# Optimization experiments

Measured on AMD Instinct MI355X. Metric: run time of the kernel, lower is better.

Reference implementation:

```python
import jax, jax.numpy as jnp
import numpy as np

N, K, D = 100000, 32, 64

def setup_inputs() -> dict:
    key = jax.random.key(0)
    k1, k2, k3 = jax.random.split(key, 3)
    x = jax.random.normal(k1, (N, D), dtype=jnp.float32)
    neighbors = jax.random.randint(k2, (N, K), 0, N, dtype=jnp.int32)
    weights = jax.random.uniform(k3, (N, K), dtype=jnp.float32)
    return {"x": x, "neighbors": neighbors, "weights": weights}

def reference(x, neighbors, weights):
    # Per-node importance pooling: normalize weights over neighbors, then
    # weighted-sum gathered neighbor features. (Vectorized form of the
    # original per-node Python loop; nodes with zero total weight keep
    # unnormalized weights, matching the `if weight_sum > 0` branch.)
    wsum = weights.sum(axis=1, keepdims=True)                 # [N, 1]
    w = jnp.where(wsum > 0, weights / wsum, weights)          # [N, K]
    nbr_feats = x[neighbors]                                  # [N, K, D] gather
    pooled = jnp.einsum("nk,nkd->nd", w, nbr_feats)          # [N, D]
    return pooled
```

## Files before the change

kernel.cpp:

```cpp
#include <hip/hip_runtime.h>
#include <hip/hip_fp16.h>


#define K_NBR 32
#define D_FEAT 64

typedef float f32x4 __attribute__((ext_vector_type(4)));
typedef unsigned int u32x2 __attribute__((ext_vector_type(2)));
typedef unsigned int u32x4 __attribute__((ext_vector_type(4)));

static __device__ __forceinline__ __half2 u32_as_h2(unsigned int u) {
  __half2 h;
  __builtin_memcpy(&h, &u, 4);
  return h;
}

static __device__ __forceinline__ unsigned int h2_as_u32(__half2 h) {
  unsigned int u;
  __builtin_memcpy(&u, &h, 4);
  return u;
}

__global__ __launch_bounds__(256) void ImportancePooling_28424093564958_convert(
    const f32x4* __restrict__ x4, u32x2* __restrict__ xh4, int n4) {
  const int i = blockIdx.x * blockDim.x + threadIdx.x;
  if (i < n4) {
    const f32x4 v = __builtin_nontemporal_load(&x4[i]);
    const __half2 a = __floats2half2_rn(v.x, v.y);
    const __half2 b = __floats2half2_rn(v.z, v.w);
    u32x2 u;
    u.x = h2_as_u32(a);
    u.y = h2_as_u32(b);
    xh4[i] = u;
  }
}

__global__ __launch_bounds__(256, 8) void ImportancePooling_28424093564958_kernel(
    const u32x4* __restrict__ xh4,
    const int* __restrict__ neighbors,
    const float* __restrict__ weights,
    f32x4* __restrict__ out4,
    int Nw) {
  const int wave_id = (int)((blockIdx.x * blockDim.x + threadIdx.x) >> 6);
  const int lane = threadIdx.x & 63;
  if (wave_id >= Nw) return;

  const int g = lane >> 3;
  const int f = lane & 7;
  const int gb4 = g << 2;
  const long hbase = (long)wave_id * 256;

  int wb[4], nb[4];
  {
    const long e0 = hbase + f * 32 + g;
    wb[0] = __float_as_int(__builtin_nontemporal_load(&weights[e0]));
    wb[1] = __float_as_int(__builtin_nontemporal_load(&weights[e0 + 8]));
    wb[2] = __float_as_int(__builtin_nontemporal_load(&weights[e0 + 16]));
    wb[3] = __float_as_int(__builtin_nontemporal_load(&weights[e0 + 24]));
    nb[0] = __builtin_nontemporal_load(&neighbors[e0]);
    nb[1] = __builtin_nontemporal_load(&neighbors[e0 + 8]);
    nb[2] = __builtin_nontemporal_load(&neighbors[e0 + 16]);
    nb[3] = __builtin_nontemporal_load(&neighbors[e0 + 24]);
  }

  float s = __int_as_float(wb[0]) + __int_as_float(wb[1]) +
            __int_as_float(wb[2]) + __int_as_float(wb[3]);
  s += __shfl_xor(s, 8, 64);
  s += __shfl_xor(s, 16, 64);
  s += __shfl_xor(s, 32, 64);
  const float invp = (s > 0.0f) ? (1.0f / s) : 1.0f;
  const float inv = __int_as_float(
      __builtin_amdgcn_ds_bpermute(gb4, __float_as_int(invp)));

  float acc[8];
#pragma unroll
  for (int i = 0; i < 8; ++i) acc[i] = 0.0f;

#pragma unroll
  for (int k = 0; k < K_NBR; ++k) {
    const int addr = ((k & 7) << 5) + gb4;
    const float wk =
        __int_as_float(__builtin_amdgcn_ds_bpermute(addr, wb[k >> 3]));
    const int idx = __builtin_amdgcn_ds_bpermute(addr, nb[k >> 3]);
    const u32x4 h = xh4[(unsigned)idx * 8u + (unsigned)f];
    const __half2 p0 = u32_as_h2(h.x);
    const __half2 p1 = u32_as_h2(h.y);
    const __half2 p2 = u32_as_h2(h.z);
    const __half2 p3 = u32_as_h2(h.w);
    acc[0] = fmaf(wk, __low2float(p0), acc[0]);
    acc[1] = fmaf(wk, __high2float(p0), acc[1]);
    acc[2] = fmaf(wk, __low2float(p1), acc[2]);
    acc[3] = fmaf(wk, __high2float(p1), acc[3]);
    acc[4] = fmaf(wk, __low2float(p2), acc[4]);
    acc[5] = fmaf(wk, __high2float(p2), acc[5]);
    acc[6] = fmaf(wk, __low2float(p3), acc[6]);
    acc[7] = fmaf(wk, __high2float(p3), acc[7]);
  }

  f32x4 o0, o1;
  o0.x = acc[0] * inv; o0.y = acc[1] * inv;
  o0.z = acc[2] * inv; o0.w = acc[3] * inv;
  o1.x = acc[4] * inv; o1.y = acc[5] * inv;
  o1.z = acc[6] * inv; o1.w = acc[7] * inv;
  const unsigned obase =
      ((unsigned)wave_id * 8u + (unsigned)g) * 16u + (unsigned)f * 2u;
  __builtin_nontemporal_store(o0, &out4[obase]);
  __builtin_nontemporal_store(o1, &out4[obase + 1]);
}

__global__ __launch_bounds__(256) void ImportancePooling_28424093564958_f32(
    const float* __restrict__ x, const int* __restrict__ neighbors,
    const float* __restrict__ weights, float* __restrict__ out, int N) {
  const int wave_id = (int)((blockIdx.x * blockDim.x + threadIdx.x) >> 6);
  const int lane = threadIdx.x & 63;
  if (wave_id >= N) return;
  const long hbase = (long)wave_id * K_NBR;
  int packed;
  if (lane < K_NBR) {
    packed = __float_as_int(weights[hbase + lane]);
  } else {
    packed = neighbors[hbase + (lane - K_NBR)];
  }
  float acc = 0.0f, wsum = 0.0f;
#pragma unroll
  for (int k = 0; k < K_NBR; ++k) {
    const float wk = __int_as_float(__builtin_amdgcn_readlane(packed, k));
    const int idx = __builtin_amdgcn_readlane(packed, K_NBR + k);
    wsum += wk;
    acc += wk * x[(long)idx * D_FEAT + lane];
  }
  const float inv = (wsum > 0.0f) ? (1.0f / wsum) : 1.0f;
  out[(long)wave_id * D_FEAT + lane] = acc * inv;
}

extern "C" void kernel_launch(void* const* d_in, const int* in_sizes, int n_in,
                              void* d_out, int out_size, void* d_ws, size_t ws_size,
                              hipStream_t stream) {
  const float* x = (const float*)d_in[0];
  const int* neighbors = (const int*)d_in[1];
  const float* weights = (const float*)d_in[2];

  const int N = in_sizes[0] / D_FEAT;
  const size_t xh_bytes = (size_t)N * D_FEAT * sizeof(__half);

  if (ws_size >= xh_bytes && (N % 8) == 0) {
    const int n4 = N * D_FEAT / 4;
    ImportancePooling_28424093564958_convert<<<(n4 + 255) / 256, 256, 0, stream>>>(
        (const f32x4*)x, (u32x2*)d_ws, n4);

    const int Nw = N / 8;
    const int block = 256;
    const int grid = (Nw * 64 + block - 1) / block;
    ImportancePooling_28424093564958_kernel<<<grid, block, 0, stream>>>(
        (const u32x4*)d_ws, neighbors, weights, (f32x4*)d_out, Nw);
  } else {
    const int block = 256;
    const int grid = (N * 64 + block - 1) / block;
    ImportancePooling_28424093564958_f32<<<grid, block, 0, stream>>>(
        x, neighbors, weights, (float*)d_out, N);
  }
}
```

Before: 150.7 us.

## Split feature gather into two half-row passes with 8-byte loads and block barrier

The main kernel now gathers each neighbor row in two passes over 32-feature halves. Each lane loads 8 bytes (four halves) per neighbor instead of 16, and only four accumulators are live. A block barrier between the passes keeps the waves of a block roughly in step, so the second-half gathers may hit cache lines brought in during the first pass. Nontemporal hints on the weight and neighbor loads and on the output stores are dropped. The trade-off is twice as many gather instructions and bpermutes, plus a synchronization point that can stall waves.

```diff
diff --git a/kernel.cpp b/kernel.cpp
--- a/kernel.cpp
+++ b/kernel.cpp
@@ -7,7 +7,6 @@
 
 typedef float f32x4 __attribute__((ext_vector_type(4)));
 typedef unsigned int u32x2 __attribute__((ext_vector_type(2)));
-typedef unsigned int u32x4 __attribute__((ext_vector_type(4)));
 
 static __device__ __forceinline__ __half2 u32_as_h2(unsigned int u) {
   __half2 h;
@@ -36,7 +35,7 @@
 }
 
 __global__ __launch_bounds__(256, 8) void ImportancePooling_28424093564958_kernel(
-    const u32x4* __restrict__ xh4,
+    const u32x2* __restrict__ xh2,
     const int* __restrict__ neighbors,
     const float* __restrict__ weights,
     f32x4* __restrict__ out4,
@@ -53,14 +52,14 @@
   int wb[4], nb[4];
   {
     const long e0 = hbase + f * 32 + g;
-    wb[0] = __float_as_int(__builtin_nontemporal_load(&weights[e0]));
-    wb[1] = __float_as_int(__builtin_nontemporal_load(&weights[e0 + 8]));
-    wb[2] = __float_as_int(__builtin_nontemporal_load(&weights[e0 + 16]));
-    wb[3] = __float_as_int(__builtin_nontemporal_load(&weights[e0 + 24]));
-    nb[0] = __builtin_nontemporal_load(&neighbors[e0]);
-    nb[1] = __builtin_nontemporal_load(&neighbors[e0 + 8]);
-    nb[2] = __builtin_nontemporal_load(&neighbors[e0 + 16]);
-    nb[3] = __builtin_nontemporal_load(&neighbors[e0 + 24]);
+    wb[0] = __float_as_int(weights[e0]);
+    wb[1] = __float_as_int(weights[e0 + 8]);
+    wb[2] = __float_as_int(weights[e0 + 16]);
+    wb[3] = __float_as_int(weights[e0 + 24]);
+    nb[0] = neighbors[e0];
+    nb[1] = neighbors[e0 + 8];
+    nb[2] = neighbors[e0 + 16];
+    nb[3] = neighbors[e0 + 24];
   }
 
   float s = __int_as_float(wb[0]) + __int_as_float(wb[1]) +
@@ -72,40 +71,32 @@
   const float inv = __int_as_float(
       __builtin_amdgcn_ds_bpermute(gb4, __float_as_int(invp)));
 
-  float acc[8];
 #pragma unroll
-  for (int i = 0; i < 8; ++i) acc[i] = 0.0f;
-
+  for (int p = 0; p < 2; ++p) {
+    float a0 = 0.0f, a1 = 0.0f, a2 = 0.0f, a3 = 0.0f;
 #pragma unroll
-  for (int k = 0; k < K_NBR; ++k) {
-    const int addr = ((k & 7) << 5) + gb4;
-    const float wk =
-        __int_as_float(__builtin_amdgcn_ds_bpermute(addr, wb[k >> 3]));
-    const int idx = __builtin_amdgcn_ds_bpermute(addr, nb[k >> 3]);
-    const u32x4 h = xh4[(unsigned)idx * 8u + (unsigned)f];
-    const __half2 p0 = u32_as_h2(h.x);
-    const __half2 p1 = u32_as_h2(h.y);
-    const __half2 p2 = u32_as_h2(h.z);
-    const __half2 p3 = u32_as_h2(h.w);
-    acc[0] = fmaf(wk, __low2float(p0), acc[0]);
-    acc[1] = fmaf(wk, __high2float(p0), acc[1]);
-    acc[2] = fmaf(wk, __low2float(p1), acc[2]);
-    acc[3] = fmaf(wk, __high2float(p1), acc[3]);
-    acc[4] = fmaf(wk, __low2float(p2), acc[4]);
-    acc[5] = fmaf(wk, __high2float(p2), acc[5]);
-    acc[6] = fmaf(wk, __low2float(p3), acc[6]);
-    acc[7] = fmaf(wk, __high2float(p3), acc[7]);
+    for (int k = 0; k < K_NBR; ++k) {
+      const int addr = ((k & 7) << 5) + gb4;
+      const float wk =
+          __int_as_float(__builtin_amdgcn_ds_bpermute(addr, wb[k >> 3]));
+      const int idx = __builtin_amdgcn_ds_bpermute(addr, nb[k >> 3]);
+      const u32x2 h = xh2[(unsigned)idx * 16u + (unsigned)(p * 8 + f)];
+      const __half2 p0 = u32_as_h2(h.x);
+      const __half2 p1 = u32_as_h2(h.y);
+      a0 = fmaf(wk, __low2float(p0), a0);
+      a1 = fmaf(wk, __high2float(p0), a1);
+      a2 = fmaf(wk, __low2float(p1), a2);
+      a3 = fmaf(wk, __high2float(p1), a3);
+    }
+    f32x4 o;
+    o.x = a0 * inv;
+    o.y = a1 * inv;
+    o.z = a2 * inv;
+    o.w = a3 * inv;
+    out4[(unsigned)wave_id * 128u + (unsigned)g * 16u + (unsigned)(p * 8 + f)] = o;
+    __builtin_amdgcn_sched_barrier(0);
+    if (p == 0) __builtin_amdgcn_s_barrier();
   }
-
-  f32x4 o0, o1;
-  o0.x = acc[0] * inv; o0.y = acc[1] * inv;
-  o0.z = acc[2] * inv; o0.w = acc[3] * inv;
-  o1.x = acc[4] * inv; o1.y = acc[5] * inv;
-  o1.z = acc[6] * inv; o1.w = acc[7] * inv;
-  const unsigned obase =
-      ((unsigned)wave_id * 8u + (unsigned)g) * 16u + (unsigned)f * 2u;
-  __builtin_nontemporal_store(o0, &out4[obase]);
-  __builtin_nontemporal_store(o1, &out4[obase + 1]);
 }
 
 __global__ __launch_bounds__(256) void ImportancePooling_28424093564958_f32(
@@ -152,7 +143,7 @@
     const int block = 256;
     const int grid = (Nw * 64 + block - 1) / block;
     ImportancePooling_28424093564958_kernel<<<grid, block, 0, stream>>>(
-        (const u32x4*)d_ws, neighbors, weights, (f32x4*)d_out, Nw);
+        (const u32x2*)d_ws, neighbors, weights, (f32x4*)d_out, Nw);
   } else {
     const int block = 256;
     const int grid = (N * 64 + block - 1) / block;
```

Measured after the change: 290.3 us. 92.7% more time.
